# Optimization experiments

Hardware: AMD Instinct MI355X
Metric: run time of the kernel (lower is better)

Reference implementation:

```python
import jax, jax.numpy as jnp
import numpy as np
from jax import lax

A = 9            # 3 scales * 3 ratios
H, W = 100, 100  # feature map
STRIDE = 16
PRE_NMS = 6000
POST_NMS = 300
NMS_THRESH = 0.7


def _make_anchors():
    """Standard py-faster-rcnn anchor grid, index order (h, w, a)."""
    base_size = 16.0
    ratios = np.array([0.5, 1.0, 2.0])
    scales = np.array([8.0, 16.0, 32.0])
    x_ctr = y_ctr = (base_size - 1.0) / 2.0
    size = base_size * base_size
    ws_r = np.round(np.sqrt(size / ratios))            # [3]
    hs_r = np.round(ws_r * ratios)                     # [3]
    ws = (ws_r[:, None] * scales[None, :]).reshape(-1)  # [9]
    hs = (hs_r[:, None] * scales[None, :]).reshape(-1)  # [9]
    base = np.stack([x_ctr - 0.5 * (ws - 1), y_ctr - 0.5 * (hs - 1),
                     x_ctr + 0.5 * (ws - 1), y_ctr + 0.5 * (hs - 1)], axis=1)  # [9,4]
    sx, sy = np.meshgrid(np.arange(W) * STRIDE, np.arange(H) * STRIDE)
    shifts = np.stack([sx.ravel(), sy.ravel(), sx.ravel(), sy.ravel()], axis=1)  # [H*W,4]
    anchors = (shifts[:, None, :] + base[None, :, :]).reshape(-1, 4)             # [H*W*A,4]
    return anchors.astype(np.float32)


def setup_inputs() -> dict:
    key = jax.random.key(0)
    k1, k2, k3 = jax.random.split(key, 3)
    return {
        "anchors": jnp.asarray(_make_anchors()),
        "rpn_cls_prob": jax.random.uniform(k1, (1, H, W, 2 * A), dtype=jnp.float32),
        "rpn_bbox_pred": jax.random.normal(k2, (1, H, W, 4 * A), dtype=jnp.float32) * 0.1,
        "rpn_trans_param": jax.random.normal(k3, (1, H, W, 6 * A), dtype=jnp.float32) * 0.1,
        "im_info": jnp.array([H * STRIDE, W * STRIDE, 1.0], dtype=jnp.float32),
    }


def _bbox_transform_inv(anchors, deltas):
    w = anchors[:, 2] - anchors[:, 0] + 1.0
    h = anchors[:, 3] - anchors[:, 1] + 1.0
    cx = anchors[:, 0] + 0.5 * w
    cy = anchors[:, 1] + 0.5 * h
    dx, dy, dw, dh = deltas[:, 0], deltas[:, 1], deltas[:, 2], deltas[:, 3]
    pcx = dx * w + cx
    pcy = dy * h + cy
    pw = jnp.exp(dw) * w
    ph = jnp.exp(dh) * h
    return jnp.stack([pcx - 0.5 * pw, pcy - 0.5 * ph,
                      pcx + 0.5 * pw, pcy + 0.5 * ph], axis=1)


def _clip_boxes(boxes, im_hw):
    im_h, im_w = im_hw[0], im_hw[1]
    x1 = jnp.clip(boxes[:, 0], 0.0, im_w - 1.0)
    y1 = jnp.clip(boxes[:, 1], 0.0, im_h - 1.0)
    x2 = jnp.clip(boxes[:, 2], 0.0, im_w - 1.0)
    y2 = jnp.clip(boxes[:, 3], 0.0, im_h - 1.0)
    return jnp.stack([x1, y1, x2, y2], axis=1)


def _nms_mask(boxes, thresh):
    """Greedy NMS on score-sorted boxes; returns keep mask [N] bool."""
    n = boxes.shape[0]
    x1, y1, x2, y2 = boxes[:, 0], boxes[:, 1], boxes[:, 2], boxes[:, 3]
    areas = (x2 - x1 + 1.0) * (y2 - y1 + 1.0)
    idx = jnp.arange(n)

    def body(i, keep):
        xx1 = jnp.maximum(x1[i], x1)
        yy1 = jnp.maximum(y1[i], y1)
        xx2 = jnp.minimum(x2[i], x2)
        yy2 = jnp.minimum(y2[i], y2)
        iw = jnp.maximum(xx2 - xx1 + 1.0, 0.0)
        ih = jnp.maximum(yy2 - yy1 + 1.0, 0.0)
        inter = iw * ih
        iou = inter / (areas[i] + areas - inter)
        suppress = (iou > thresh) & (idx > i) & keep[i]
        return keep & (~suppress)

    return lax.fori_loop(0, n, body, jnp.ones((n,), dtype=bool))


def _forward(anchors, rpn_cls_prob, rpn_bbox_pred, rpn_trans_param, im_info):
    scores = rpn_cls_prob[:, :, :, A:].reshape(-1)      # fg probs, order (h,w,a)
    deltas = rpn_bbox_pred.reshape(-1, 4)
    trans = rpn_trans_param.reshape(-1, 6)

    proposals = _bbox_transform_inv(anchors, deltas)
    proposals = _clip_boxes(proposals, im_info[:2])

    order = jnp.argsort(-scores)[:PRE_NMS]
    scores = scores[order]
    proposals = proposals[order]
    trans = trans[order]

    keep = _nms_mask(proposals, NMS_THRESH)
    # fixed-size keep indices (score-descending order preserved); padded with 0
    keep_idx = jnp.where(keep, size=POST_NMS, fill_value=0)[0]

    proposals = proposals[keep_idx]
    scores = scores[keep_idx]
    trans = trans[keep_idx]

    batch_inds = jnp.zeros((proposals.shape[0], 1), dtype=proposals.dtype)
    blob = jnp.concatenate([batch_inds, proposals], axis=1)  # [POST_NMS, 5]
    return blob, scores, trans


def reference(anchors, rpn_cls_prob, rpn_bbox_pred, rpn_trans_param, im_info):
    return _forward(anchors, rpn_cls_prob, rpn_bbox_pred, rpn_trans_param, im_info)
```

## Files before the change

### kernel.cpp

```cpp
#include <hip/hip_runtime.h>
#include <stdint.h>
#include <math.h>

#define A_ 9
#define N_ANCH 90000
#define PRE_NMS 6000
#define POST_NMS 300
#define NMS_TH 0.7f
#define NBINS 4096
#define SLOT_CAP 64
#define RANK_BINS 512
#define MASK_W 94
#define CAPC 16
#define MW2 16
#define NTILE2 136

#define OFF_BCNT   0u
#define OFF_BUCKET 16384u
#define OFF_ORDER  2113536u
#define OFF_TSCORE 2137536u
#define OFF_TBOX   2161536u
#define OFF_MASK   2257536u

typedef unsigned long long u64;
typedef unsigned int u32;

__device__ __forceinline__ int score_bin(float s) {
    int bin = (int)(s * (float)NBINS);
    return bin < 0 ? 0 : (bin > NBINS - 1 ? NBINS - 1 : bin);
}

__global__ void __launch_bounds__(256) k_zero(int4* __restrict__ bcnt4) {
#pragma unroll
    for (int k = 0; k < 4; ++k)
        bcnt4[k * 256 + threadIdx.x] = make_int4(0, 0, 0, 0);
}

__global__ void k_scatter(const float* __restrict__ cls,
                          int* __restrict__ bucketCnt,
                          u64* __restrict__ buckets) {
    int n = blockIdx.x * blockDim.x + threadIdx.x;
    if (n >= N_ANCH) return;
    float s = cls[(n / A_) * (2 * A_) + A_ + (n % A_)];
    int bin = score_bin(s);
    int slot = atomicAdd(&bucketCnt[bin], 1);
    if (slot < SLOT_CAP) {
        u64 key = ((u64)__float_as_uint(s) << 32) | (u64)(0xFFFFFFFFu - (u32)n);
        buckets[(size_t)bin * SLOT_CAP + slot] = key;
    }
}

__device__ __forceinline__ int block_scan(const int* __restrict__ hist,
                                          int* sufs, int* sfx, int* tsh,
                                          int hl[16]) {
    int t = threadIdx.x;
    int csum = 0;
#pragma unroll
    for (int k = 0; k < 16; ++k) { hl[k] = hist[t * 16 + k]; csum += hl[k]; }
    sfx[t] = csum;
    if (t == 0) *tsh = 0;
    __syncthreads();
    for (int off = 1; off < 256; off <<= 1) {
        int v = (t + off < 256) ? sfx[t + off] : 0;
        __syncthreads();
        sfx[t] += v;
        __syncthreads();
    }
    int acc = sfx[t] - csum;
    int best = -1;
#pragma unroll
    for (int k = 15; k >= 0; --k) {
        sufs[t * 16 + k] = acc;
        acc += hl[k];
        if (best < 0 && acc >= PRE_NMS) best = t * 16 + k;
    }
    if (best >= 0) atomicMax(tsh, best);
    __syncthreads();
    return *tsh;
}

__global__ void __launch_bounds__(256) k_rank(const u64* __restrict__ buckets,
                                              const int* __restrict__ bucketCnt,
                                              const float* __restrict__ anchors,
                                              const float* __restrict__ bbox,
                                              const float* __restrict__ im_info,
                                              int* __restrict__ order,
                                              float* __restrict__ tscore,
                                              float* __restrict__ tb) {
#pragma clang fp contract(off)
    __shared__ int sufs[NBINS];
    __shared__ int sfx[256];
    __shared__ int tsh;
    int hl[16];
    int T = block_scan(bucketCnt, sufs, sfx, &tsh, hl);
    int gid = blockIdx.x * 256 + threadIdx.x;
    int bin = (NBINS - RANK_BINS) + (gid >> 6);
    int slot = gid & (SLOT_CAP - 1);
    if (bin < T) return;
    int cnt = bucketCnt[bin];
    if (cnt > SLOT_CAP) cnt = SLOT_CAP;
    if (slot >= cnt) return;
    const u64* bk = buckets + (size_t)bin * SLOT_CAP;
    u64 ki = bk[slot];
    int rank = sufs[bin];
    for (int j = 0; j < cnt; ++j)
        rank += (bk[j] > ki) ? 1 : 0;
    if (rank >= PRE_NMS) return;

    int n = (int)(0xFFFFFFFFu - (u32)(ki & 0xFFFFFFFFull));
    order[rank] = n;
    tscore[rank] = __uint_as_float((u32)(ki >> 32));

    int hw = n / A_, a = n % A_;
    const float* an = anchors + (size_t)n * 4;
    const float* d  = bbox + (size_t)hw * (4 * A_) + a * 4;
    float w  = an[2] - an[0] + 1.0f;
    float h  = an[3] - an[1] + 1.0f;
    float cx = an[0] + 0.5f * w;
    float cy = an[1] + 0.5f * h;
    float pcx = d[0] * w + cx;
    float pcy = d[1] * h + cy;
    float pw  = expf(d[2]) * w;
    float ph  = expf(d[3]) * h;
    float x1 = pcx - 0.5f * pw;
    float y1 = pcy - 0.5f * ph;
    float x2 = pcx + 0.5f * pw;
    float y2 = pcy + 0.5f * ph;
    float im_h = im_info[0], im_w = im_info[1];
    x1 = fminf(fmaxf(x1, 0.0f), im_w - 1.0f);
    y1 = fminf(fmaxf(y1, 0.0f), im_h - 1.0f);
    x2 = fminf(fmaxf(x2, 0.0f), im_w - 1.0f);
    y2 = fminf(fmaxf(y2, 0.0f), im_h - 1.0f);
    tb[rank * 4 + 0] = x1;
    tb[rank * 4 + 1] = y1;
    tb[rank * 4 + 2] = x2;
    tb[rank * 4 + 3] = y2;
}

__device__ __forceinline__ bool iou_gt(float4 rb, float ra, float4 cb, float ca) {
#pragma clang fp contract(off)
    float xx1 = fmaxf(rb.x, cb.x);
    float yy1 = fmaxf(rb.y, cb.y);
    float xx2 = fminf(rb.z, cb.z);
    float yy2 = fminf(rb.w, cb.w);
    float iw = fmaxf(xx2 - xx1 + 1.0f, 0.0f);
    float ih = fmaxf(yy2 - yy1 + 1.0f, 0.0f);
    float inter = iw * ih;
    return inter / (ra + ca - inter) > NMS_TH;
}

__global__ void __launch_bounds__(64) k_mask(const float* __restrict__ tb,
                                             u64* __restrict__ mask) {
#pragma clang fp contract(off)
    int t5 = (int)blockIdx.x;
    int cb = 0;
    while ((cb + 1) * (cb + 2) / 2 <= t5) ++cb;
    int rb = t5 - cb * (cb + 1) / 2;

    __shared__ float cbx[64][4];
    __shared__ float car[64];
    int t = threadIdx.x;
    int j0 = cb * 64;
    int jj = j0 + t;
    {
        float bx1 = tb[jj * 4 + 0], by1 = tb[jj * 4 + 1];
        float bx2 = tb[jj * 4 + 2], by2 = tb[jj * 4 + 3];
        cbx[t][0] = bx1; cbx[t][1] = by1; cbx[t][2] = bx2; cbx[t][3] = by2;
        car[t] = (bx2 - bx1 + 1.0f) * (by2 - by1 + 1.0f);
    }
    __syncthreads();
    int row = rb * 64 + t;
    float x1 = tb[row * 4 + 0], y1 = tb[row * 4 + 1];
    float x2 = tb[row * 4 + 2], y2 = tb[row * 4 + 3];
    float ai = (x2 - x1 + 1.0f) * (y2 - y1 + 1.0f);
    u64 bits = 0;
    for (int c = 0; c < 64; ++c) {
        int j = j0 + c;
        if (j > row) {
            float xx1 = fmaxf(x1, cbx[c][0]);
            float yy1 = fmaxf(y1, cbx[c][1]);
            float xx2 = fminf(x2, cbx[c][2]);
            float yy2 = fminf(y2, cbx[c][3]);
            float iw = fmaxf(xx2 - xx1 + 1.0f, 0.0f);
            float ih = fmaxf(yy2 - yy1 + 1.0f, 0.0f);
            float inter = iw * ih;
            float iou = inter / (ai + car[c] - inter);
            if (iou > NMS_TH) bits |= (1ull << c);
        }
    }
    mask[(size_t)row * MW2 + cb] = bits;
}

__global__ void __launch_bounds__(256)
k_reduce_out(const u64* __restrict__ mask, const float4* __restrict__ tb4,
             const int* __restrict__ order, const float* __restrict__ tscore,
             const float* __restrict__ trans, float* __restrict__ out) {
#pragma clang fp contract(off)
    __shared__ int keep_s[POST_NMS];
    __shared__ int ctrl[2];
    __shared__ u64 curq[4];
    __shared__ u64 sdg[64];
    const int t = threadIdx.x;
    const int lane = t & 63, wq = t >> 6;

    if (t < 64) {
        int cnt = 0;
        u64 cur = 0;
        u64 dwc = mask[(size_t)lane * MW2 + 0];
        int done = 0;
        for (int c = 0; c < CAPC; ++c) {
            int nc = c + 1;
            u64 dwn = 0;
            if (nc < CAPC) dwn = mask[(size_t)(nc * 64 + lane) * MW2 + nc];
            u32 dlo_v = (u32)dwc, dhi_v = (u32)(dwc >> 32);
            int cnt0 = cnt;
            u64 keptw = 0;
            u64 freeb = ~cur;
            while (freeb != 0ull && cnt < POST_NMS) {
                u32 bs;
                asm("s_ff1_i32_b64 %0, %1" : "=s"(bs) : "s"(freeb));
                u32 dlo, dhi;
                asm("v_readlane_b32 %0, %1, %2" : "=s"(dlo) : "v"(dlo_v), "s"(bs));
                asm("v_readlane_b32 %0, %1, %2" : "=s"(dhi) : "v"(dhi_v), "s"(bs));
                u64 bit = 1ull << bs;
                keptw |= bit;
                cur |= (((u64)dhi << 32) | (u64)dlo) | bit;
                cnt++;
                freeb = ~cur;
            }
            if ((keptw >> lane) & 1ull) {
                int pos = cnt0 + __popcll(keptw & ((1ull << lane) - 1ull));
                keep_s[pos] = c * 64 + lane;
            }
            if (cnt >= POST_NMS) { done = 1; break; }
            if (nc >= CAPC) break;
            u64 acc = 0;
#pragma unroll
            for (int s = 0; s < 5; ++s) {
                int p = s * 64 + lane;
                if (p < cnt) acc |= mask[(size_t)keep_s[p] * MW2 + nc];
            }
#pragma unroll
            for (int m = 32; m >= 1; m >>= 1)
                acc |= (u64)__shfl_xor((unsigned long long)acc, m, 64);
            u32 clo = __builtin_amdgcn_readfirstlane((u32)acc);
            u32 chi = __builtin_amdgcn_readfirstlane((u32)(acc >> 32));
            cur = ((u64)chi << 32) | (u64)clo;
            dwc = dwn;
        }
        if (lane == 0) { ctrl[0] = cnt; ctrl[1] = done; }
    }
    __syncthreads();

    int cnt = ctrl[0];
    if (!ctrl[1]) {
        for (int c = CAPC; c < MASK_W && cnt < POST_NMS; ++c) {
            int jg = c * 64 + lane;
            bool jvalid = jg < PRE_NMS;
            float4 bj = make_float4(0.0f, 0.0f, -2.0f, -2.0f);
            float aj = 1.0f;
            if (jvalid) { bj = tb4[jg]; aj = (bj.z - bj.x + 1.0f) * (bj.w - bj.y + 1.0f); }
            bool sup = false;
            for (int k = wq; k < cnt; k += 4) {
                int r = keep_s[k];
                float4 br = tb4[r];
                float ar2 = (br.z - br.x + 1.0f) * (br.w - br.y + 1.0f);
                if (jvalid) sup = sup || iou_gt(br, ar2, bj, aj);
            }
            u64 bw = __ballot((int)sup);
            if (lane == 0) curq[wq] = bw;
            if (t < 64) {
                u64 bits = 0;
                if (jvalid) {
                    for (int cc = t + 1; cc < 64; ++cc) {
                        int j2 = c * 64 + cc;
                        if (j2 < PRE_NMS) {
                            float4 cb2 = tb4[j2];
                            float ca2 = (cb2.z - cb2.x + 1.0f) * (cb2.w - cb2.y + 1.0f);
                            if (iou_gt(bj, aj, cb2, ca2)) bits |= 1ull << cc;
                        }
                    }
                }
                sdg[t] = bits;
            }
            __syncthreads();
            if (t < 64) {
                u64 cur = curq[0] | curq[1] | curq[2] | curq[3];
                u64 dwc = sdg[lane];
                int nrows = PRE_NMS - c * 64; if (nrows > 64) nrows = 64;
                u64 vm = (nrows >= 64) ? ~0ull : ((1ull << nrows) - 1ull);
                u32 dlo_v = (u32)dwc, dhi_v = (u32)(dwc >> 32);
                int cnt0 = cnt;
                u64 keptw = 0;
                u64 freeb = (~cur) & vm;
                while (freeb != 0ull && cnt < POST_NMS) {
                    u32 bs = __builtin_amdgcn_readfirstlane((u32)__builtin_ctzll(freeb));
                    u32 dlo, dhi;
                    asm("v_readlane_b32 %0, %1, %2" : "=s"(dlo) : "v"(dlo_v), "s"(bs));
                    asm("v_readlane_b32 %0, %1, %2" : "=s"(dhi) : "v"(dhi_v), "s"(bs));
                    u64 bit = 1ull << bs;
                    keptw |= bit;
                    cur |= (((u64)dhi << 32) | (u64)dlo) | bit;
                    cnt++;
                    freeb = (~cur) & vm;
                }
                if ((keptw >> lane) & 1ull) {
                    int pos = cnt0 + __popcll(keptw & ((1ull << lane) - 1ull));
                    keep_s[pos] = c * 64 + lane;
                }
                if (lane == 0) {
                    ctrl[0] = cnt;
                    ctrl[1] = (cnt >= POST_NMS) ? 1 : 0;
                }
            }
            __syncthreads();
            cnt = ctrl[0];
            if (ctrl[1]) break;
        }
    }

    for (int r = cnt + t; r < POST_NMS; r += 256) keep_s[r] = 0;
    __syncthreads();
    const float* tbf = (const float*)tb4;
    for (int row = t; row < POST_NMS; row += 256) {
        int r = keep_s[row];
        int n = order[r];
        out[row * 5 + 0] = 0.0f;
        out[row * 5 + 1] = tbf[r * 4 + 0];
        out[row * 5 + 2] = tbf[r * 4 + 1];
        out[row * 5 + 3] = tbf[r * 4 + 2];
        out[row * 5 + 4] = tbf[r * 4 + 3];
        out[POST_NMS * 5 + row] = tscore[r];
        int hw = n / A_, a = n % A_;
        const float* tp = trans + (size_t)hw * (6 * A_) + a * 6;
#pragma unroll
        for (int cc = 0; cc < 6; ++cc)
            out[POST_NMS * 6 + row * 6 + cc] = tp[cc];
    }
}

extern "C" void kernel_launch(void* const* d_in, const int* in_sizes, int n_in,
                              void* d_out, int out_size, void* d_ws, size_t ws_size,
                              hipStream_t stream) {
    const float* anchors = (const float*)d_in[0];
    const float* cls     = (const float*)d_in[1];
    const float* bbox    = (const float*)d_in[2];
    const float* trans   = (const float*)d_in[3];
    const float* im_info = (const float*)d_in[4];
    float* out = (float*)d_out;
    char* ws = (char*)d_ws;

    int*   bcnt    = (int*)(ws + OFF_BCNT);
    u64*   buckets = (u64*)(ws + OFF_BUCKET);
    int*   order   = (int*)(ws + OFF_ORDER);
    float* tscore  = (float*)(ws + OFF_TSCORE);
    float* tb      = (float*)(ws + OFF_TBOX);
    u64*   mask    = (u64*)(ws + OFF_MASK);

    int nb = (N_ANCH + 255) / 256;
    k_zero<<<1, 256, 0, stream>>>((int4*)bcnt);
    k_scatter<<<nb, 256, 0, stream>>>(cls, bcnt, buckets);
    k_rank<<<(RANK_BINS * SLOT_CAP) / 256, 256, 0, stream>>>(buckets, bcnt,
                                                             anchors, bbox, im_info,
                                                             order, tscore, tb);
    k_mask<<<NTILE2, 64, 0, stream>>>(tb, mask);
    k_reduce_out<<<1, 256, 0, stream>>>(mask, (const float4*)tb,
                                        order, tscore, trans, out);
}
```

Before: 60.37 us.

## Fuse rank, mask and reduce kernels into one flag-synchronized persistent launch

```diff
diff --git a/kernel.cpp b/kernel.cpp
--- a/kernel.cpp
+++ b/kernel.cpp
@@ -14,6 +14,8 @@
 #define CAPC 16
 #define MW2 16
 #define NTILE2 136
+#define NRANKBLK 128
+#define NMASKBLK 34
 
 #define OFF_BCNT   0u
 #define OFF_BUCKET 16384u
@@ -21,6 +23,7 @@
 #define OFF_TSCORE 2137536u
 #define OFF_TBOX   2161536u
 #define OFF_MASK   2257536u
+#define OFF_FLAGS  2388608u
 
 typedef unsigned long long u64;
 typedef unsigned int u32;
@@ -30,10 +33,12 @@
     return bin < 0 ? 0 : (bin > NBINS - 1 ? NBINS - 1 : bin);
 }
 
-__global__ void __launch_bounds__(256) k_zero(int4* __restrict__ bcnt4) {
+__global__ void __launch_bounds__(256) k_zero(char* __restrict__ ws) {
+    int4* bcnt4 = (int4*)(ws + OFF_BCNT);
 #pragma unroll
     for (int k = 0; k < 4; ++k)
         bcnt4[k * 256 + threadIdx.x] = make_int4(0, 0, 0, 0);
+    if (threadIdx.x < 2) ((int*)(ws + OFF_FLAGS))[threadIdx.x] = 0;
 }
 
 __global__ void k_scatter(const float* __restrict__ cls,
@@ -79,64 +84,6 @@
     return *tsh;
 }
 
-__global__ void __launch_bounds__(256) k_rank(const u64* __restrict__ buckets,
-                                              const int* __restrict__ bucketCnt,
-                                              const float* __restrict__ anchors,
-                                              const float* __restrict__ bbox,
-                                              const float* __restrict__ im_info,
-                                              int* __restrict__ order,
-                                              float* __restrict__ tscore,
-                                              float* __restrict__ tb) {
-#pragma clang fp contract(off)
-    __shared__ int sufs[NBINS];
-    __shared__ int sfx[256];
-    __shared__ int tsh;
-    int hl[16];
-    int T = block_scan(bucketCnt, sufs, sfx, &tsh, hl);
-    int gid = blockIdx.x * 256 + threadIdx.x;
-    int bin = (NBINS - RANK_BINS) + (gid >> 6);
-    int slot = gid & (SLOT_CAP - 1);
-    if (bin < T) return;
-    int cnt = bucketCnt[bin];
-    if (cnt > SLOT_CAP) cnt = SLOT_CAP;
-    if (slot >= cnt) return;
-    const u64* bk = buckets + (size_t)bin * SLOT_CAP;
-    u64 ki = bk[slot];
-    int rank = sufs[bin];
-    for (int j = 0; j < cnt; ++j)
-        rank += (bk[j] > ki) ? 1 : 0;
-    if (rank >= PRE_NMS) return;
-
-    int n = (int)(0xFFFFFFFFu - (u32)(ki & 0xFFFFFFFFull));
-    order[rank] = n;
-    tscore[rank] = __uint_as_float((u32)(ki >> 32));
-
-    int hw = n / A_, a = n % A_;
-    const float* an = anchors + (size_t)n * 4;
-    const float* d  = bbox + (size_t)hw * (4 * A_) + a * 4;
-    float w  = an[2] - an[0] + 1.0f;
-    float h  = an[3] - an[1] + 1.0f;
-    float cx = an[0] + 0.5f * w;
-    float cy = an[1] + 0.5f * h;
-    float pcx = d[0] * w + cx;
-    float pcy = d[1] * h + cy;
-    float pw  = expf(d[2]) * w;
-    float ph  = expf(d[3]) * h;
-    float x1 = pcx - 0.5f * pw;
-    float y1 = pcy - 0.5f * ph;
-    float x2 = pcx + 0.5f * pw;
-    float y2 = pcy + 0.5f * ph;
-    float im_h = im_info[0], im_w = im_info[1];
-    x1 = fminf(fmaxf(x1, 0.0f), im_w - 1.0f);
-    y1 = fminf(fmaxf(y1, 0.0f), im_h - 1.0f);
-    x2 = fminf(fmaxf(x2, 0.0f), im_w - 1.0f);
-    y2 = fminf(fmaxf(y2, 0.0f), im_h - 1.0f);
-    tb[rank * 4 + 0] = x1;
-    tb[rank * 4 + 1] = y1;
-    tb[rank * 4 + 2] = x2;
-    tb[rank * 4 + 3] = y2;
-}
-
 __device__ __forceinline__ bool iou_gt(float4 rb, float ra, float4 cb, float ca) {
 #pragma clang fp contract(off)
     float xx1 = fmaxf(rb.x, cb.x);
@@ -149,59 +96,136 @@
     return inter / (ra + ca - inter) > NMS_TH;
 }
 
-__global__ void __launch_bounds__(64) k_mask(const float* __restrict__ tb,
-                                             u64* __restrict__ mask) {
+__global__ void __launch_bounds__(256)
+k_pipeline(const u64* __restrict__ buckets, const int* __restrict__ bucketCnt,
+           const float* __restrict__ anchors, const float* __restrict__ bbox,
+           const float* __restrict__ im_info, int* __restrict__ order,
+           float* __restrict__ tscore, float* __restrict__ tb,
+           u64* __restrict__ mask, int* __restrict__ flags,
+           const float* __restrict__ trans, float* __restrict__ out) {
 #pragma clang fp contract(off)
-    int t5 = (int)blockIdx.x;
-    int cb = 0;
-    while ((cb + 1) * (cb + 2) / 2 <= t5) ++cb;
-    int rb = t5 - cb * (cb + 1) / 2;
-
-    __shared__ float cbx[64][4];
-    __shared__ float car[64];
-    int t = threadIdx.x;
-    int j0 = cb * 64;
-    int jj = j0 + t;
-    {
-        float bx1 = tb[jj * 4 + 0], by1 = tb[jj * 4 + 1];
-        float bx2 = tb[jj * 4 + 2], by2 = tb[jj * 4 + 3];
-        cbx[t][0] = bx1; cbx[t][1] = by1; cbx[t][2] = bx2; cbx[t][3] = by2;
-        car[t] = (bx2 - bx1 + 1.0f) * (by2 - by1 + 1.0f);
-    }
-    __syncthreads();
-    int row = rb * 64 + t;
-    float x1 = tb[row * 4 + 0], y1 = tb[row * 4 + 1];
-    float x2 = tb[row * 4 + 2], y2 = tb[row * 4 + 3];
-    float ai = (x2 - x1 + 1.0f) * (y2 - y1 + 1.0f);
-    u64 bits = 0;
-    for (int c = 0; c < 64; ++c) {
-        int j = j0 + c;
-        if (j > row) {
-            float xx1 = fmaxf(x1, cbx[c][0]);
-            float yy1 = fmaxf(y1, cbx[c][1]);
-            float xx2 = fminf(x2, cbx[c][2]);
-            float yy2 = fminf(y2, cbx[c][3]);
-            float iw = fmaxf(xx2 - xx1 + 1.0f, 0.0f);
-            float ih = fmaxf(yy2 - yy1 + 1.0f, 0.0f);
-            float inter = iw * ih;
-            float iou = inter / (ai + car[c] - inter);
-            if (iou > NMS_TH) bits |= (1ull << c);
-        }
-    }
-    mask[(size_t)row * MW2 + cb] = bits;
-}
-
-__global__ void __launch_bounds__(256)
-k_reduce_out(const u64* __restrict__ mask, const float4* __restrict__ tb4,
-             const int* __restrict__ order, const float* __restrict__ tscore,
-             const float* __restrict__ trans, float* __restrict__ out) {
-#pragma clang fp contract(off)
+    const int b = (int)blockIdx.x;
+    const int t = threadIdx.x;
+
+    if (b >= 1 && b <= NRANKBLK) {
+        __shared__ int sufs[NBINS];
+        __shared__ int sfx[256];
+        __shared__ int tsh;
+        int hl[16];
+        int T = block_scan(bucketCnt, sufs, sfx, &tsh, hl);
+        int gid = (b - 1) * 256 + t;
+        int bin = (NBINS - RANK_BINS) + (gid >> 6);
+        int slot = gid & (SLOT_CAP - 1);
+        if (bin >= T) {
+            int cnt = bucketCnt[bin];
+            if (cnt > SLOT_CAP) cnt = SLOT_CAP;
+            if (slot < cnt) {
+                const u64* bk = buckets + (size_t)bin * SLOT_CAP;
+                u64 ki = bk[slot];
+                int rank = sufs[bin];
+                for (int j = 0; j < cnt; ++j)
+                    rank += (bk[j] > ki) ? 1 : 0;
+                if (rank < PRE_NMS) {
+                    int n = (int)(0xFFFFFFFFu - (u32)(ki & 0xFFFFFFFFull));
+                    order[rank] = n;
+                    tscore[rank] = __uint_as_float((u32)(ki >> 32));
+                    int hw = n / A_, a = n % A_;
+                    const float* an = anchors + (size_t)n * 4;
+                    const float* d  = bbox + (size_t)hw * (4 * A_) + a * 4;
+                    float w  = an[2] - an[0] + 1.0f;
+                    float h  = an[3] - an[1] + 1.0f;
+                    float cx = an[0] + 0.5f * w;
+                    float cy = an[1] + 0.5f * h;
+                    float pcx = d[0] * w + cx;
+                    float pcy = d[1] * h + cy;
+                    float pw  = expf(d[2]) * w;
+                    float ph  = expf(d[3]) * h;
+                    float x1 = pcx - 0.5f * pw;
+                    float y1 = pcy - 0.5f * ph;
+                    float x2 = pcx + 0.5f * pw;
+                    float y2 = pcy + 0.5f * ph;
+                    float im_h = im_info[0], im_w = im_info[1];
+                    x1 = fminf(fmaxf(x1, 0.0f), im_w - 1.0f);
+                    y1 = fminf(fmaxf(y1, 0.0f), im_h - 1.0f);
+                    x2 = fminf(fmaxf(x2, 0.0f), im_w - 1.0f);
+                    y2 = fminf(fmaxf(y2, 0.0f), im_h - 1.0f);
+                    tb[rank * 4 + 0] = x1;
+                    tb[rank * 4 + 1] = y1;
+                    tb[rank * 4 + 2] = x2;
+                    tb[rank * 4 + 3] = y2;
+                }
+            }
+        }
+        __syncthreads();
+        if (t == 0) {
+            __threadfence();
+            __hip_atomic_fetch_add(&flags[0], 1, __ATOMIC_RELEASE,
+                                   __HIP_MEMORY_SCOPE_AGENT);
+        }
+        return;
+    }
+
+    if (b > NRANKBLK) {
+        __shared__ float sbx[4][64][5];
+        const int wq = t >> 6, lane = t & 63;
+        int t5 = (b - NRANKBLK - 1) * 4 + wq;
+        while (__hip_atomic_load(&flags[0], __ATOMIC_ACQUIRE,
+                                 __HIP_MEMORY_SCOPE_AGENT) < NRANKBLK) {}
+        int cb = 0, rb = 0;
+        if (t5 < NTILE2) {
+            cb = 0;
+            while ((cb + 1) * (cb + 2) / 2 <= t5) ++cb;
+            rb = t5 - cb * (cb + 1) / 2;
+            int jj = cb * 64 + lane;
+            float bx1 = tb[jj * 4 + 0], by1 = tb[jj * 4 + 1];
+            float bx2 = tb[jj * 4 + 2], by2 = tb[jj * 4 + 3];
+            sbx[wq][lane][0] = bx1; sbx[wq][lane][1] = by1;
+            sbx[wq][lane][2] = bx2; sbx[wq][lane][3] = by2;
+            sbx[wq][lane][4] = (bx2 - bx1 + 1.0f) * (by2 - by1 + 1.0f);
+        }
+        __syncthreads();
+        if (t5 < NTILE2) {
+            int row = rb * 64 + lane;
+            float x1 = tb[row * 4 + 0], y1 = tb[row * 4 + 1];
+            float x2 = tb[row * 4 + 2], y2 = tb[row * 4 + 3];
+            float ai = (x2 - x1 + 1.0f) * (y2 - y1 + 1.0f);
+            int j0 = cb * 64;
+            u64 bits = 0;
+            for (int c = 0; c < 64; ++c) {
+                int j = j0 + c;
+                if (j > row) {
+                    float xx1 = fmaxf(x1, sbx[wq][c][0]);
+                    float yy1 = fmaxf(y1, sbx[wq][c][1]);
+                    float xx2 = fminf(x2, sbx[wq][c][2]);
+                    float yy2 = fminf(y2, sbx[wq][c][3]);
+                    float iw = fmaxf(xx2 - xx1 + 1.0f, 0.0f);
+                    float ih = fmaxf(yy2 - yy1 + 1.0f, 0.0f);
+                    float inter = iw * ih;
+                    float iou = inter / (ai + sbx[wq][c][4] - inter);
+                    if (iou > NMS_TH) bits |= (1ull << c);
+                }
+            }
+            mask[(size_t)row * MW2 + cb] = bits;
+        }
+        __syncthreads();
+        if (t == 0) {
+            __threadfence();
+            __hip_atomic_fetch_add(&flags[1], 1, __ATOMIC_RELEASE,
+                                   __HIP_MEMORY_SCOPE_AGENT);
+        }
+        return;
+    }
+
     __shared__ int keep_s[POST_NMS];
     __shared__ int ctrl[2];
     __shared__ u64 curq[4];
     __shared__ u64 sdg[64];
-    const int t = threadIdx.x;
     const int lane = t & 63, wq = t >> 6;
+    const float4* tb4 = (const float4*)tb;
+
+    while (__hip_atomic_load(&flags[1], __ATOMIC_ACQUIRE,
+                             __HIP_MEMORY_SCOPE_AGENT) < NMASKBLK) {}
+    __syncthreads();
 
     if (t < 64) {
         int cnt = 0;
@@ -321,15 +345,14 @@
 
     for (int r = cnt + t; r < POST_NMS; r += 256) keep_s[r] = 0;
     __syncthreads();
-    const float* tbf = (const float*)tb4;
     for (int row = t; row < POST_NMS; row += 256) {
         int r = keep_s[row];
         int n = order[r];
         out[row * 5 + 0] = 0.0f;
-        out[row * 5 + 1] = tbf[r * 4 + 0];
-        out[row * 5 + 2] = tbf[r * 4 + 1];
-        out[row * 5 + 3] = tbf[r * 4 + 2];
-        out[row * 5 + 4] = tbf[r * 4 + 3];
+        out[row * 5 + 1] = tb[r * 4 + 0];
+        out[row * 5 + 2] = tb[r * 4 + 1];
+        out[row * 5 + 3] = tb[r * 4 + 2];
+        out[row * 5 + 4] = tb[r * 4 + 3];
         out[POST_NMS * 5 + row] = tscore[r];
         int hw = n / A_, a = n % A_;
         const float* tp = trans + (size_t)hw * (6 * A_) + a * 6;
@@ -356,14 +379,12 @@
     float* tscore  = (float*)(ws + OFF_TSCORE);
     float* tb      = (float*)(ws + OFF_TBOX);
     u64*   mask    = (u64*)(ws + OFF_MASK);
+    int*   flags   = (int*)(ws + OFF_FLAGS);
 
     int nb = (N_ANCH + 255) / 256;
-    k_zero<<<1, 256, 0, stream>>>((int4*)bcnt);
+    k_zero<<<1, 256, 0, stream>>>(ws);
     k_scatter<<<nb, 256, 0, stream>>>(cls, bcnt, buckets);
-    k_rank<<<(RANK_BINS * SLOT_CAP) / 256, 256, 0, stream>>>(buckets, bcnt,
-                                                             anchors, bbox, im_info,
-                                                             order, tscore, tb);
-    k_mask<<<NTILE2, 64, 0, stream>>>(tb, mask);
-    k_reduce_out<<<1, 256, 0, stream>>>(mask, (const float4*)tb,
-                                        order, tscore, trans, out);
-}
+    k_pipeline<<<1 + NRANKBLK + NMASKBLK, 256, 0, stream>>>(
+        buckets, bcnt, anchors, bbox, im_info, order, tscore, tb,
+        mask, flags, trans, out);
+}
```

Result: slower. 68.34 us (+13.2%).

## Fuse NMS mask build into reduce kernel and restrict rank scan to top bins

Applied to the files above, without the earlier changes.

```diff
diff --git a/kernel.cpp b/kernel.cpp
--- a/kernel.cpp
+++ b/kernel.cpp
@@ -10,17 +10,17 @@
 #define NBINS 4096
 #define SLOT_CAP 64
 #define RANK_BINS 512
+#define BASE_BIN (NBINS - RANK_BINS)
 #define MASK_W 94
-#define CAPC 16
-#define MW2 16
-#define NTILE2 136
+#define CAPC 9
+#define WROWS (CAPC * 64)
+#define NT0 (CAPC * (CAPC + 1) / 2)
 
 #define OFF_BCNT   0u
 #define OFF_BUCKET 16384u
 #define OFF_ORDER  2113536u
 #define OFF_TSCORE 2137536u
 #define OFF_TBOX   2161536u
-#define OFF_MASK   2257536u
 
 typedef unsigned long long u64;
 typedef unsigned int u32;
@@ -50,35 +50,6 @@
     }
 }
 
-__device__ __forceinline__ int block_scan(const int* __restrict__ hist,
-                                          int* sufs, int* sfx, int* tsh,
-                                          int hl[16]) {
-    int t = threadIdx.x;
-    int csum = 0;
-#pragma unroll
-    for (int k = 0; k < 16; ++k) { hl[k] = hist[t * 16 + k]; csum += hl[k]; }
-    sfx[t] = csum;
-    if (t == 0) *tsh = 0;
-    __syncthreads();
-    for (int off = 1; off < 256; off <<= 1) {
-        int v = (t + off < 256) ? sfx[t + off] : 0;
-        __syncthreads();
-        sfx[t] += v;
-        __syncthreads();
-    }
-    int acc = sfx[t] - csum;
-    int best = -1;
-#pragma unroll
-    for (int k = 15; k >= 0; --k) {
-        sufs[t * 16 + k] = acc;
-        acc += hl[k];
-        if (best < 0 && acc >= PRE_NMS) best = t * 16 + k;
-    }
-    if (best >= 0) atomicMax(tsh, best);
-    __syncthreads();
-    return *tsh;
-}
-
 __global__ void __launch_bounds__(256) k_rank(const u64* __restrict__ buckets,
                                               const int* __restrict__ bucketCnt,
                                               const float* __restrict__ anchors,
@@ -88,21 +59,46 @@
                                               float* __restrict__ tscore,
                                               float* __restrict__ tb) {
 #pragma clang fp contract(off)
-    __shared__ int sufs[NBINS];
+    __shared__ int sufs[RANK_BINS];
     __shared__ int sfx[256];
     __shared__ int tsh;
-    int hl[16];
-    int T = block_scan(bucketCnt, sufs, sfx, &tsh, hl);
-    int gid = blockIdx.x * 256 + threadIdx.x;
-    int bin = (NBINS - RANK_BINS) + (gid >> 6);
+    int t = threadIdx.x;
+    int hl[2];
+    hl[0] = bucketCnt[BASE_BIN + t * 2];
+    hl[1] = bucketCnt[BASE_BIN + t * 2 + 1];
+    int csum = hl[0] + hl[1];
+    sfx[t] = csum;
+    if (t == 0) tsh = 0;
+    __syncthreads();
+    for (int off = 1; off < 256; off <<= 1) {
+        int v = (t + off < 256) ? sfx[t + off] : 0;
+        __syncthreads();
+        sfx[t] += v;
+        __syncthreads();
+    }
+    int acc = sfx[t] - csum;
+    int best = -1;
+#pragma unroll
+    for (int k = 1; k >= 0; --k) {
+        sufs[t * 2 + k] = acc;
+        acc += hl[k];
+        if (best < 0 && acc >= PRE_NMS) best = t * 2 + k;
+    }
+    if (best >= 0) atomicMax(&tsh, best);
+    __syncthreads();
+    int Tl = tsh;
+
+    int gid = blockIdx.x * 256 + t;
+    int lb = gid >> 6;
     int slot = gid & (SLOT_CAP - 1);
-    if (bin < T) return;
+    if (lb < Tl) return;
+    int bin = BASE_BIN + lb;
     int cnt = bucketCnt[bin];
     if (cnt > SLOT_CAP) cnt = SLOT_CAP;
     if (slot >= cnt) return;
     const u64* bk = buckets + (size_t)bin * SLOT_CAP;
     u64 ki = bk[slot];
-    int rank = sufs[bin];
+    int rank = sufs[lb];
     for (int j = 0; j < cnt; ++j)
         rank += (bk[j] > ki) ? 1 : 0;
     if (rank >= PRE_NMS) return;
@@ -149,69 +145,54 @@
     return inter / (ra + ca - inter) > NMS_TH;
 }
 
-__global__ void __launch_bounds__(64) k_mask(const float* __restrict__ tb,
-                                             u64* __restrict__ mask) {
+__global__ void __launch_bounds__(256)
+k_reduce_out(const float4* __restrict__ tb4, const int* __restrict__ order,
+             const float* __restrict__ tscore, const float* __restrict__ trans,
+             float* __restrict__ out) {
 #pragma clang fp contract(off)
-    int t5 = (int)blockIdx.x;
-    int cb = 0;
-    while ((cb + 1) * (cb + 2) / 2 <= t5) ++cb;
-    int rb = t5 - cb * (cb + 1) / 2;
-
-    __shared__ float cbx[64][4];
-    __shared__ float car[64];
-    int t = threadIdx.x;
-    int j0 = cb * 64;
-    int jj = j0 + t;
-    {
-        float bx1 = tb[jj * 4 + 0], by1 = tb[jj * 4 + 1];
-        float bx2 = tb[jj * 4 + 2], by2 = tb[jj * 4 + 3];
-        cbx[t][0] = bx1; cbx[t][1] = by1; cbx[t][2] = bx2; cbx[t][3] = by2;
-        car[t] = (bx2 - bx1 + 1.0f) * (by2 - by1 + 1.0f);
-    }
-    __syncthreads();
-    int row = rb * 64 + t;
-    float x1 = tb[row * 4 + 0], y1 = tb[row * 4 + 1];
-    float x2 = tb[row * 4 + 2], y2 = tb[row * 4 + 3];
-    float ai = (x2 - x1 + 1.0f) * (y2 - y1 + 1.0f);
-    u64 bits = 0;
-    for (int c = 0; c < 64; ++c) {
-        int j = j0 + c;
-        if (j > row) {
-            float xx1 = fmaxf(x1, cbx[c][0]);
-            float yy1 = fmaxf(y1, cbx[c][1]);
-            float xx2 = fminf(x2, cbx[c][2]);
-            float yy2 = fminf(y2, cbx[c][3]);
-            float iw = fmaxf(xx2 - xx1 + 1.0f, 0.0f);
-            float ih = fmaxf(yy2 - yy1 + 1.0f, 0.0f);
-            float inter = iw * ih;
-            float iou = inter / (ai + car[c] - inter);
-            if (iou > NMS_TH) bits |= (1ull << c);
-        }
-    }
-    mask[(size_t)row * MW2 + cb] = bits;
-}
-
-__global__ void __launch_bounds__(256)
-k_reduce_out(const u64* __restrict__ mask, const float4* __restrict__ tb4,
-             const int* __restrict__ order, const float* __restrict__ tscore,
-             const float* __restrict__ trans, float* __restrict__ out) {
-#pragma clang fp contract(off)
-    __shared__ int keep_s[POST_NMS];
-    __shared__ int ctrl[2];
-    __shared__ u64 curq[4];
-    __shared__ u64 sdg[64];
+    __shared__ float4 sbox[WROWS];
+    __shared__ float  sarea[WROWS];
+    __shared__ u64    smask[WROWS][CAPC];
+    __shared__ int    keep_s[POST_NMS];
+    __shared__ int    ctrl[2];
+    __shared__ u64    curq[4];
+    __shared__ u64    sdg[64];
     const int t = threadIdx.x;
     const int lane = t & 63, wq = t >> 6;
+
+    for (int i = t; i < WROWS; i += 256) {
+        float4 b = tb4[i];
+        sbox[i] = b;
+        sarea[i] = (b.z - b.x + 1.0f) * (b.w - b.y + 1.0f);
+    }
+    __syncthreads();
+    for (int g = t; g < NT0 * 64; g += 256) {
+        int tile = g >> 6, ri = g & 63;
+        int cb = 0;
+        while ((cb + 1) * (cb + 2) / 2 <= tile) ++cb;
+        int rb = tile - cb * (cb + 1) / 2;
+        int row = rb * 64 + ri;
+        int j0 = cb * 64;
+        float4 rbx = sbox[row];
+        float ra = sarea[row];
+        u64 bits = 0;
+        for (int c = 0; c < 64; ++c) {
+            int j = j0 + c;
+            if (j > row && iou_gt(rbx, ra, sbox[j], sarea[j])) bits |= 1ull << c;
+        }
+        smask[row][cb] = bits;
+    }
+    __syncthreads();
 
     if (t < 64) {
         int cnt = 0;
         u64 cur = 0;
-        u64 dwc = mask[(size_t)lane * MW2 + 0];
+        u64 dwc = smask[lane][0];
         int done = 0;
         for (int c = 0; c < CAPC; ++c) {
             int nc = c + 1;
             u64 dwn = 0;
-            if (nc < CAPC) dwn = mask[(size_t)(nc * 64 + lane) * MW2 + nc];
+            if (nc < CAPC) dwn = smask[nc * 64 + lane][nc];
             u32 dlo_v = (u32)dwc, dhi_v = (u32)(dwc >> 32);
             int cnt0 = cnt;
             u64 keptw = 0;
@@ -238,7 +219,7 @@
 #pragma unroll
             for (int s = 0; s < 5; ++s) {
                 int p = s * 64 + lane;
-                if (p < cnt) acc |= mask[(size_t)keep_s[p] * MW2 + nc];
+                if (p < cnt) acc |= smask[keep_s[p]][nc];
             }
 #pragma unroll
             for (int m = 32; m >= 1; m >>= 1)
@@ -355,7 +336,6 @@
     int*   order   = (int*)(ws + OFF_ORDER);
     float* tscore  = (float*)(ws + OFF_TSCORE);
     float* tb      = (float*)(ws + OFF_TBOX);
-    u64*   mask    = (u64*)(ws + OFF_MASK);
 
     int nb = (N_ANCH + 255) / 256;
     k_zero<<<1, 256, 0, stream>>>((int4*)bcnt);
@@ -363,7 +343,5 @@
     k_rank<<<(RANK_BINS * SLOT_CAP) / 256, 256, 0, stream>>>(buckets, bcnt,
                                                              anchors, bbox, im_info,
                                                              order, tscore, tb);
-    k_mask<<<NTILE2, 64, 0, stream>>>(tb, mask);
-    k_reduce_out<<<1, 256, 0, stream>>>(mask, (const float4*)tb,
-                                        order, tscore, trans, out);
-}
+    k_reduce_out<<<1, 256, 0, stream>>>((const float4*)tb, order, tscore, trans, out);
+}
```

New measurement: 152.8 us. 2.53x slower.
